# Optimization experiments

Hardware: AMD Instinct MI355X
Metric: run time of the kernel (lower is better)

The kernel has to match this reference:

```python
import jax, jax.numpy as jnp
import numpy as np

TEMP = 13.544
EPS = 1e-5  # BatchNorm2d default eps


def setup_inputs() -> dict:
    key = jax.random.key(0)
    k1, = jax.random.split(key, 1)
    N, S, E = 16, 1024, 512
    x = jax.random.normal(k1, (N, S, E), dtype=jnp.float32)
    gamma = jnp.ones((1,), dtype=jnp.float32)   # BatchNorm2d(1).weight
    beta = jnp.zeros((1,), dtype=jnp.float32)   # BatchNorm2d(1).bias
    return {"x": x, "gamma": gamma, "beta": beta}


def reference(x, gamma, beta):
    # Pairwise squared L2 distances via GEMM identity:
    # ||a-b||^2 = ||a||^2 + ||b||^2 - 2 a.b   (symmetric, matches the
    # original broadcast diff+square+sum without the O(S^2 E) intermediate)
    sq = jnp.sum(x * x, axis=-1)                    # (N, S)
    gram = jnp.einsum('bse,bte->bst', x, x)         # (N, S, S)
    d = sq[:, :, None] + sq[:, None, :] - 2.0 * gram  # (N, S, S)
    d = jnp.maximum(d, 0.0)                          # numerical floor (exact math is >= 0)

    # BatchNorm2d(1) in training mode: stats over all elements of the single channel
    d = d[:, None, :, :]                             # (N, 1, S, S)
    mean = jnp.mean(d)
    var = jnp.mean((d - mean) ** 2)                  # biased variance, as torch uses for normalization
    d_hat = (d - mean) * jax.lax.rsqrt(var + EPS)
    out = d_hat * gamma.reshape(1, 1, 1, 1) + beta.reshape(1, 1, 1, 1)

    # softmax(-out / 13.544) over last dim
    return jax.nn.softmax(-out / TEMP, axis=-1)      # (N, 1, S, S)
```

## Files before the change

kernel.cpp:

```cpp
#include <hip/hip_runtime.h>
#include <hip/hip_bf16.h>


#define S_DIM 1024
#define E_DIM 512
#define NBATCH 16
#define NSTEP2 (E_DIM / 64)
#define TEMP_C 13.544

typedef __attribute__((ext_vector_type(4))) float f32x4;
typedef __attribute__((ext_vector_type(8))) short bf16x8;
typedef __attribute__((ext_vector_type(8))) _Float16 f16x8;

__device__ inline unsigned pkbf(float lo, float hi) {
  unsigned a = __float_as_uint(lo), b = __float_as_uint(hi);
  a = (a + 0x7FFFu + ((a >> 16) & 1u)) >> 16;
  b = (b + 0x7FFFu + ((b >> 16) & 1u)) & 0xFFFF0000u;
  return b | a;
}

__device__ inline void gload16(const void* g, void* l) {
  __builtin_amdgcn_global_load_lds(
      (const __attribute__((address_space(1))) unsigned*)g,
      (__attribute__((address_space(3))) unsigned*)l, 16, 0, 0);
}

__global__ __launch_bounds__(256) void sqcvt(const float* __restrict__ x,
                                             ushort* __restrict__ xb16,
                                             float* __restrict__ sq,
                                             double* __restrict__ sums) {
  const int wave = threadIdx.x >> 6, lane = threadIdx.x & 63;
  const size_t row = (size_t)blockIdx.x * 4 + wave;
  const float4* xr = reinterpret_cast<const float4*>(x + row * E_DIM);
  float4 a = xr[lane * 2], b = xr[lane * 2 + 1];
  uint4 p;
  p.x = pkbf(a.x, a.y); p.y = pkbf(a.z, a.w);
  p.z = pkbf(b.x, b.y); p.w = pkbf(b.z, b.w);
  *reinterpret_cast<uint4*>(xb16 + row * E_DIM + lane * 8) = p;
  float s = a.x*a.x + a.y*a.y + a.z*a.z + a.w*a.w +
            b.x*b.x + b.y*b.y + b.z*b.z + b.w*b.w;
#pragma unroll
  for (int o = 32; o > 0; o >>= 1) s += __shfl_xor(s, o);
  if (lane == 0) sq[row] = s;
  if (blockIdx.x == 0 && threadIdx.x == 0) { sums[0] = 0.0; sums[1] = 0.0; }
}

template <int MODE>
__global__ __launch_bounds__(512, 2) void gram6(const ushort* __restrict__ xb16,
                                                const float* __restrict__ sq,
                                                float* __restrict__ dout,
                                                _Float16* __restrict__ dp,
                                                double* __restrict__ sums) {
  __shared__ ushort lA[2][2][8192];
  __shared__ ushort lB[2][2][8192];
  __shared__ double red[16];

  const int tid = threadIdx.x, wave = tid >> 6, lane = tid & 63;
  const int wr = wave >> 2, wc = wave & 3;

  const int bid = blockIdx.x;
  const int xcd = bid & 7, j = bid >> 3;
  const int b = xcd * 2 + (j >> 4);
  const int tile = j & 15;
  const int tr = tile >> 2, tc = tile & 3;

  const ushort* xb = xb16 + (size_t)b * (S_DIM * E_DIM);
  const int rowA0 = tr * 256, rowB0 = tc * 256;

  int eA[2], eB[2];
#pragma unroll
  for (int i = 0; i < 2; ++i) {
    int p = i * 512 + tid;
    int r = p >> 2;
    int s = (p & 3) ^ ((r >> 1) & 3);
    eA[i] = (rowA0 + r) * E_DIM + s * 8;
    eB[i] = (rowB0 + r) * E_DIM + s * 8;
  }

  auto stage = [&](int buf, int k0) {
#pragma unroll
    for (int c = 0; c < 2; ++c) {
      char* la = (char*)&lA[buf][c][0];
      char* lb = (char*)&lB[buf][c][0];
      gload16(xb + eA[0] + k0 + c * 32, la + tid * 16);
      gload16(xb + eA[1] + k0 + c * 32, la + 8192 + tid * 16);
      gload16(xb + eB[0] + k0 + c * 32, lb + tid * 16);
      gload16(xb + eB[1] + k0 + c * 32, lb + 8192 + tid * 16);
    }
  };

  f32x4 acc[8][4] = {};

  stage(0, 0);
  int buf = 0;
#pragma unroll 1
  for (int ks = 0; ks < NSTEP2; ++ks) {
    __syncthreads();
    if (ks + 1 < NSTEP2) stage(buf ^ 1, (ks + 1) * 64);
#pragma unroll
    for (int c = 0; c < 2; ++c) {
      bf16x8 af[8], bfr[4];
      const int s0 = lane >> 4;
      const char* la = (const char*)&lA[buf][c][0];
      const char* lb = (const char*)&lB[buf][c][0];
#pragma unroll
      for (int m = 0; m < 8; ++m) {
        int row = wr * 128 + m * 16 + (lane & 15);
        af[m] = *reinterpret_cast<const bf16x8*>(la + row * 64 + ((s0 ^ ((row >> 1) & 3)) << 4));
      }
#pragma unroll
      for (int n = 0; n < 4; ++n) {
        int row = wc * 64 + n * 16 + (lane & 15);
        bfr[n] = *reinterpret_cast<const bf16x8*>(lb + row * 64 + ((s0 ^ ((row >> 1) & 3)) << 4));
      }
#pragma unroll
      for (int m = 0; m < 8; ++m)
#pragma unroll
        for (int n = 0; n < 4; ++n)
          acc[m][n] = __builtin_amdgcn_mfma_f32_16x16x32_bf16(af[m], bfr[n], acc[m][n], 0, 0, 0);
    }
    buf ^= 1;
  }

  const float* sqb = sq + b * S_DIM;
  double sd = 0.0, sd2 = 0.0;
#pragma unroll
  for (int m = 0; m < 8; ++m) {
    int gr0 = tr * 256 + wr * 128 + m * 16 + ((lane >> 4) << 2);
    float sqr0 = sqb[gr0], sqr1 = sqb[gr0 + 1], sqr2 = sqb[gr0 + 2], sqr3 = sqb[gr0 + 3];
#pragma unroll
    for (int n = 0; n < 4; ++n) {
      int gc = tc * 256 + wc * 64 + n * 16 + (lane & 15);
      float sqc = sqb[gc];
      float d0 = fmaxf(sqr0 + sqc - 2.0f * acc[m][n][0], 0.0f);
      float d1 = fmaxf(sqr1 + sqc - 2.0f * acc[m][n][1], 0.0f);
      float d2 = fmaxf(sqr2 + sqc - 2.0f * acc[m][n][2], 0.0f);
      float d3 = fmaxf(sqr3 + sqc - 2.0f * acc[m][n][3], 0.0f);
      if (MODE == 0) {
        float* dbase = dout + (size_t)b * S_DIM * S_DIM;
        dbase[(size_t)(gr0 + 0) * S_DIM + gc] = d0;
        dbase[(size_t)(gr0 + 1) * S_DIM + gc] = d1;
        dbase[(size_t)(gr0 + 2) * S_DIM + gc] = d2;
        dbase[(size_t)(gr0 + 3) * S_DIM + gc] = d3;
      } else {
        _Float16* dbase = dp + (size_t)b * S_DIM * S_DIM;
        dbase[(size_t)(gr0 + 0) * S_DIM + gc] = (_Float16)(d0 - sqr0);
        dbase[(size_t)(gr0 + 1) * S_DIM + gc] = (_Float16)(d1 - sqr1);
        dbase[(size_t)(gr0 + 2) * S_DIM + gc] = (_Float16)(d2 - sqr2);
        dbase[(size_t)(gr0 + 3) * S_DIM + gc] = (_Float16)(d3 - sqr3);
      }
      sd += (double)d0 + (double)d1 + (double)d2 + (double)d3;
      sd2 += (double)d0 * d0 + (double)d1 * d1 + (double)d2 * d2 + (double)d3 * d3;
    }
  }
#pragma unroll
  for (int o = 32; o > 0; o >>= 1) {
    sd += __shfl_xor(sd, o);
    sd2 += __shfl_xor(sd2, o);
  }
  if (lane == 0) { red[wave] = sd; red[8 + wave] = sd2; }
  __syncthreads();
  if (tid == 0) {
    double t1 = 0.0, t2 = 0.0;
#pragma unroll
    for (int w = 0; w < 8; ++w) { t1 += red[w]; t2 += red[8 + w]; }
    atomicAdd(&sums[0], t1);
    atomicAdd(&sums[1], t2);
  }
}

__device__ inline float ln_scale(const double* sums, const float* gamma) {
  constexpr double invN = 1.0 / (16.0 * 1024.0 * 1024.0);
  double mean = sums[0] * invN;
  double var = sums[1] * invN - mean * mean;
  return (float)(-((double)gamma[0]) / (sqrt(var + 1e-5) * TEMP_C));
}

__global__ __launch_bounds__(256) void softmax_f32(float* __restrict__ d,
                                                   const double* __restrict__ sums,
                                                   const float* __restrict__ gamma) {
  const int wave = threadIdx.x >> 6, lane = threadIdx.x & 63;
  const size_t row = (size_t)blockIdx.x * 4 + wave;
  const float scale = ln_scale(sums, gamma);
  float4* r4 = reinterpret_cast<float4*>(d + row * S_DIM);
  float4 v[4];
#pragma unroll
  for (int i = 0; i < 4; ++i) v[i] = r4[lane + 64 * i];
  float l[16];
#pragma unroll
  for (int i = 0; i < 4; ++i) {
    l[4*i+0] = scale * v[i].x; l[4*i+1] = scale * v[i].y;
    l[4*i+2] = scale * v[i].z; l[4*i+3] = scale * v[i].w;
  }
  float mx = l[0];
#pragma unroll
  for (int i = 1; i < 16; ++i) mx = fmaxf(mx, l[i]);
#pragma unroll
  for (int o = 32; o > 0; o >>= 1) mx = fmaxf(mx, __shfl_xor(mx, o));
  const float L2E = 1.4426950408889634f;
  float e[16], s = 0.f;
#pragma unroll
  for (int i = 0; i < 16; ++i) { e[i] = exp2f((l[i] - mx) * L2E); s += e[i]; }
#pragma unroll
  for (int o = 32; o > 0; o >>= 1) s += __shfl_xor(s, o);
  float inv = 1.0f / s;
#pragma unroll
  for (int i = 0; i < 4; ++i)
    r4[lane + 64 * i] = make_float4(e[4*i]*inv, e[4*i+1]*inv, e[4*i+2]*inv, e[4*i+3]*inv);
}

__global__ __launch_bounds__(256) void softmax_f16(const _Float16* __restrict__ dp,
                                                   float* __restrict__ out,
                                                   const double* __restrict__ sums,
                                                   const float* __restrict__ gamma) {
  const int wave = threadIdx.x >> 6, lane = threadIdx.x & 63;
  const size_t row = (size_t)blockIdx.x * 4 + wave;
  const float scale = ln_scale(sums, gamma);
  const f16x8* r8 = reinterpret_cast<const f16x8*>(dp + row * S_DIM);
  f16x8 h0 = r8[lane * 2], h1 = r8[lane * 2 + 1];
  float l[16];
#pragma unroll
  for (int i = 0; i < 8; ++i) { l[i] = scale * (float)h0[i]; l[8 + i] = scale * (float)h1[i]; }
  float mx = l[0];
#pragma unroll
  for (int i = 1; i < 16; ++i) mx = fmaxf(mx, l[i]);
#pragma unroll
  for (int o = 32; o > 0; o >>= 1) mx = fmaxf(mx, __shfl_xor(mx, o));
  const float L2E = 1.4426950408889634f;
  float e[16], s = 0.f;
#pragma unroll
  for (int i = 0; i < 16; ++i) { e[i] = exp2f((l[i] - mx) * L2E); s += e[i]; }
#pragma unroll
  for (int o = 32; o > 0; o >>= 1) s += __shfl_xor(s, o);
  float inv = 1.0f / s;
  float4* o4 = reinterpret_cast<float4*>(out + row * S_DIM);
#pragma unroll
  for (int i = 0; i < 4; ++i)
    o4[lane * 4 + i] = make_float4(e[4*i]*inv, e[4*i+1]*inv, e[4*i+2]*inv, e[4*i+3]*inv);
}

extern "C" void kernel_launch(void* const* d_in, const int* in_sizes, int n_in,
                              void* d_out, int out_size, void* d_ws, size_t ws_size,
                              hipStream_t stream) {
  const float* x = (const float*)d_in[0];
  const float* gamma = (const float*)d_in[1];
  float* out = (float*)d_out;
  double* sums = (double*)d_ws;
  float* sq = (float*)((char*)d_ws + 256);
  ushort* xb16 = (ushort*)((char*)d_ws + 256 + 65536);
  _Float16* dp = (_Float16*)((char*)d_ws + 256 + 65536 +
                             (size_t)NBATCH * S_DIM * E_DIM * 2);
  const size_t need_b = 256 + 65536 + (size_t)NBATCH * S_DIM * E_DIM * 2;
  const size_t need_a = need_b + (size_t)NBATCH * S_DIM * S_DIM * 2;

  sqcvt<<<dim3(NBATCH * S_DIM / 4), dim3(256), 0, stream>>>(x, xb16, sq, sums);
  if (ws_size >= need_a) {
    gram6<1><<<dim3(256), dim3(512), 0, stream>>>(xb16, sq, out, dp, sums);
    softmax_f16<<<dim3(NBATCH * S_DIM / 4), dim3(256), 0, stream>>>(dp, out, sums, gamma);
  } else {
    gram6<0><<<dim3(256), dim3(512), 0, stream>>>(xb16, sq, out, dp, sums);
    softmax_f32<<<dim3(NBATCH * S_DIM / 4), dim3(256), 0, stream>>>(out, sums, gamma);
  }
}
```

Baseline: 143.3 us.

## Load GEMM fragments directly from global memory and remap rows by XCD

The gram kernel no longer stages A/B tiles through double-buffered LDS with global_load_lds. Each wave now reads its bf16 MFMA fragments straight from global memory (L2-cached), which removes the barriers and LDS traffic and frees LDS for occupancy. The sqcvt and softmax kernels remap block index to row so that each XCD handles a contiguous batch range, matching the gram kernel's XCD-to-batch mapping for L2 locality. The cost is redundant global/L2 reads across waves that previously shared an LDS tile, and exposed memory latency with no explicit prefetch.

```diff
diff --git a/kernel.cpp b/kernel.cpp
--- a/kernel.cpp
+++ b/kernel.cpp
@@ -5,7 +5,6 @@
 #define S_DIM 1024
 #define E_DIM 512
 #define NBATCH 16
-#define NSTEP2 (E_DIM / 64)
 #define TEMP_C 13.544
 
 typedef __attribute__((ext_vector_type(4))) float f32x4;
@@ -19,18 +18,13 @@
   return b | a;
 }
 
-__device__ inline void gload16(const void* g, void* l) {
-  __builtin_amdgcn_global_load_lds(
-      (const __attribute__((address_space(1))) unsigned*)g,
-      (__attribute__((address_space(3))) unsigned*)l, 16, 0, 0);
-}
-
 __global__ __launch_bounds__(256) void sqcvt(const float* __restrict__ x,
                                              ushort* __restrict__ xb16,
                                              float* __restrict__ sq,
                                              double* __restrict__ sums) {
   const int wave = threadIdx.x >> 6, lane = threadIdx.x & 63;
-  const size_t row = (size_t)blockIdx.x * 4 + wave;
+  const int xcd = blockIdx.x & 7, li = blockIdx.x >> 3;
+  const size_t row = (size_t)xcd * 2048 + (size_t)li * 4 + wave;
   const float4* xr = reinterpret_cast<const float4*>(x + row * E_DIM);
   float4 a = xr[lane * 2], b = xr[lane * 2 + 1];
   uint4 p;
@@ -46,13 +40,11 @@
 }
 
 template <int MODE>
-__global__ __launch_bounds__(512, 2) void gram6(const ushort* __restrict__ xb16,
-                                                const float* __restrict__ sq,
-                                                float* __restrict__ dout,
-                                                _Float16* __restrict__ dp,
-                                                double* __restrict__ sums) {
-  __shared__ ushort lA[2][2][8192];
-  __shared__ ushort lB[2][2][8192];
+__global__ __launch_bounds__(512) void gram8(const ushort* __restrict__ xb16,
+                                             const float* __restrict__ sq,
+                                             float* __restrict__ dout,
+                                             _Float16* __restrict__ dp,
+                                             double* __restrict__ sums) {
   __shared__ double red[16];
 
   const int tid = threadIdx.x, wave = tid >> 6, lane = tid & 63;
@@ -67,59 +59,28 @@
   const ushort* xb = xb16 + (size_t)b * (S_DIM * E_DIM);
   const int rowA0 = tr * 256, rowB0 = tc * 256;
 
-  int eA[2], eB[2];
-#pragma unroll
-  for (int i = 0; i < 2; ++i) {
-    int p = i * 512 + tid;
-    int r = p >> 2;
-    int s = (p & 3) ^ ((r >> 1) & 3);
-    eA[i] = (rowA0 + r) * E_DIM + s * 8;
-    eB[i] = (rowB0 + r) * E_DIM + s * 8;
-  }
-
-  auto stage = [&](int buf, int k0) {
-#pragma unroll
-    for (int c = 0; c < 2; ++c) {
-      char* la = (char*)&lA[buf][c][0];
-      char* lb = (char*)&lB[buf][c][0];
-      gload16(xb + eA[0] + k0 + c * 32, la + tid * 16);
-      gload16(xb + eA[1] + k0 + c * 32, la + 8192 + tid * 16);
-      gload16(xb + eB[0] + k0 + c * 32, lb + tid * 16);
-      gload16(xb + eB[1] + k0 + c * 32, lb + 8192 + tid * 16);
-    }
-  };
+  const char* Abase = (const char*)(xb + (size_t)(rowA0 + wr * 128 + (lane & 15)) * E_DIM)
+                      + (lane >> 4) * 16;
+  const char* Bbase = (const char*)(xb + (size_t)(rowB0 + wc * 64 + (lane & 15)) * E_DIM)
+                      + (lane >> 4) * 16;
 
   f32x4 acc[8][4] = {};
 
-  stage(0, 0);
-  int buf = 0;
-#pragma unroll 1
-  for (int ks = 0; ks < NSTEP2; ++ks) {
-    __syncthreads();
-    if (ks + 1 < NSTEP2) stage(buf ^ 1, (ks + 1) * 64);
-#pragma unroll
-    for (int c = 0; c < 2; ++c) {
-      bf16x8 af[8], bfr[4];
-      const int s0 = lane >> 4;
-      const char* la = (const char*)&lA[buf][c][0];
-      const char* lb = (const char*)&lB[buf][c][0];
-#pragma unroll
-      for (int m = 0; m < 8; ++m) {
-        int row = wr * 128 + m * 16 + (lane & 15);
-        af[m] = *reinterpret_cast<const bf16x8*>(la + row * 64 + ((s0 ^ ((row >> 1) & 3)) << 4));
-      }
-#pragma unroll
-      for (int n = 0; n < 4; ++n) {
-        int row = wc * 64 + n * 16 + (lane & 15);
-        bfr[n] = *reinterpret_cast<const bf16x8*>(lb + row * 64 + ((s0 ^ ((row >> 1) & 3)) << 4));
-      }
-#pragma unroll
-      for (int m = 0; m < 8; ++m)
-#pragma unroll
-        for (int n = 0; n < 4; ++n)
-          acc[m][n] = __builtin_amdgcn_mfma_f32_16x16x32_bf16(af[m], bfr[n], acc[m][n], 0, 0, 0);
-    }
-    buf ^= 1;
+#pragma unroll 2
+  for (int ks = 0; ks < E_DIM / 32; ++ks) {
+    const int ko = ks * 64;
+    bf16x8 af[8], bfr[4];
+#pragma unroll
+    for (int m = 0; m < 8; ++m)
+      af[m] = *reinterpret_cast<const bf16x8*>(Abase + (size_t)m * 16 * 1024 + ko);
+#pragma unroll
+    for (int n = 0; n < 4; ++n)
+      bfr[n] = *reinterpret_cast<const bf16x8*>(Bbase + (size_t)n * 16 * 1024 + ko);
+#pragma unroll
+    for (int m = 0; m < 8; ++m)
+#pragma unroll
+      for (int n = 0; n < 4; ++n)
+        acc[m][n] = __builtin_amdgcn_mfma_f32_16x16x32_bf16(af[m], bfr[n], acc[m][n], 0, 0, 0);
   }
 
   const float* sqb = sq + b * S_DIM;
@@ -180,7 +141,8 @@
                                                    const double* __restrict__ sums,
                                                    const float* __restrict__ gamma) {
   const int wave = threadIdx.x >> 6, lane = threadIdx.x & 63;
-  const size_t row = (size_t)blockIdx.x * 4 + wave;
+  const int xcd = blockIdx.x & 7, li = blockIdx.x >> 3;
+  const size_t row = (size_t)xcd * 2048 + (size_t)li * 4 + wave;
   const float scale = ln_scale(sums, gamma);
   float4* r4 = reinterpret_cast<float4*>(d + row * S_DIM);
   float4 v[4];
@@ -214,7 +176,8 @@
                                                    const double* __restrict__ sums,
                                                    const float* __restrict__ gamma) {
   const int wave = threadIdx.x >> 6, lane = threadIdx.x & 63;
-  const size_t row = (size_t)blockIdx.x * 4 + wave;
+  const int xcd = blockIdx.x & 7, li = blockIdx.x >> 3;
+  const size_t row = (size_t)xcd * 2048 + (size_t)li * 4 + wave;
   const float scale = ln_scale(sums, gamma);
   const f16x8* r8 = reinterpret_cast<const f16x8*>(dp + row * S_DIM);
   f16x8 h0 = r8[lane * 2], h1 = r8[lane * 2 + 1];
@@ -255,10 +218,10 @@
 
   sqcvt<<<dim3(NBATCH * S_DIM / 4), dim3(256), 0, stream>>>(x, xb16, sq, sums);
   if (ws_size >= need_a) {
-    gram6<1><<<dim3(256), dim3(512), 0, stream>>>(xb16, sq, out, dp, sums);
+    gram8<1><<<dim3(256), dim3(512), 0, stream>>>(xb16, sq, out, dp, sums);
     softmax_f16<<<dim3(NBATCH * S_DIM / 4), dim3(256), 0, stream>>>(dp, out, sums, gamma);
   } else {
-    gram6<0><<<dim3(256), dim3(512), 0, stream>>>(xb16, sq, out, dp, sums);
+    gram8<0><<<dim3(256), dim3(512), 0, stream>>>(xb16, sq, out, dp, sums);
     softmax_f32<<<dim3(NBATCH * S_DIM / 4), dim3(256), 0, stream>>>(out, sums, gamma);
   }
 }
```

New measurement: 175.0 us. 1.22x slower.
